# Kernel tuning notes

Hardware: AMD Instinct MI355X
Metric: run time of the kernel (lower is better)

The kernel has to match this reference:

```python
import jax, jax.numpy as jnp
import numpy as np


def _analytic_phase(x):
    """FFT-based analytic-signal phase, mean over channels. x: (B, C, T) -> (B, T)."""
    B, C, T = x.shape
    Xf = jnp.fft.fft(x, axis=-1)  # complex64
    # Hilbert multiplier: h[0]=1, h[1:T//2]=2, h[T//2]=1 (T even), rest 0
    h = np.zeros((T,), dtype=np.float32)
    h[0] = 1.0
    h[1:T // 2] = 2.0
    if T % 2 == 0:
        h[T // 2] = 1.0
    analytic = jnp.fft.ifft(Xf * jnp.asarray(h), axis=-1)
    phase = jnp.angle(analytic)          # (B, C, T)
    return phase.mean(axis=1)            # (B, T)


def setup_inputs() -> dict:
    key = jax.random.key(0)
    k = jax.random.split(key, 6)
    B, C, T = 32, 9, 4096
    num_codes, code_dim = 512, 64
    half = code_dim // 2
    s = 1.0 / np.sqrt(C)  # kaiming-uniform-ish scale for Linear(9, .)
    return {
        "imu_signal": jax.random.normal(k[0], (B, C, T), dtype=jnp.float32),
        "W_mag": jax.random.uniform(k[1], (half, C), jnp.float32, -s, s),
        "b_mag": jax.random.uniform(k[2], (half,), jnp.float32, -s, s),
        "W_phase": jax.random.uniform(k[3], (half, C), jnp.float32, -s, s),
        "b_phase": jax.random.uniform(k[4], (half,), jnp.float32, -s, s),
        "codebook": jax.random.normal(k[5], (num_codes, code_dim), dtype=jnp.float32),
    }


def reference(imu_signal, W_mag, b_mag, W_phase, b_phase, codebook):
    # imu_signal: (B, 9, T)
    phases = _analytic_phase(imu_signal)                      # (B, T)
    imu_btc = jnp.transpose(imu_signal, (0, 2, 1))            # (B, T, 9)

    mag_features = imu_btc @ W_mag.T + b_mag                  # (B, T, 32)

    phase_input = jnp.stack([jnp.cos(phases), jnp.sin(phases)], axis=-1)  # (B, T, 2)
    combined = jnp.concatenate([imu_btc[:, :, :7], phase_input], axis=-1)  # (B, T, 9)
    phase_features = combined @ W_phase.T + b_phase           # (B, T, 32)

    features = jnp.concatenate([mag_features, phase_features], axis=-1)  # (B, T, 64)

    # cdist argmin == argmin of squared distances: ||f||^2 - 2 f.c + ||c||^2
    d2 = (jnp.sum(features * features, axis=-1, keepdims=True)
          - 2.0 * jnp.einsum("btd,kd->btk", features, codebook)
          + jnp.sum(codebook * codebook, axis=-1))            # (B, T, K)
    indices = jnp.argmin(d2, axis=-1)                         # (B, T)
    quantized = codebook[indices]                             # (B, T, 64)
    return quantized, indices, phases
```

## Files before the change

kernel.cpp:

```cpp
#include <hip/hip_runtime.h>
#include <math.h>

#define TN 4096
#define HN 2048
#define NB 32
#define NCH 9
#define NCODES 512
#define CDIM 64
#define TAU 1e-3f
#define PTS 256
#define CHK 128
#define NCHK 4
#define VQT 512

typedef _Float16 f16x8 __attribute__((ext_vector_type(8)));
typedef float f32x4 __attribute__((ext_vector_type(4)));

__device__ __forceinline__ float2 cmulf(float2 a, float2 b) {
    return make_float2(a.x * b.x - a.y * b.y, a.x * b.y + a.y * b.x);
}
__device__ __forceinline__ float2 f2add(float2 a, float2 b) {
    return make_float2(a.x + b.x, a.y + b.y);
}
__device__ __forceinline__ float2 f2sub(float2 a, float2 b) {
    return make_float2(a.x - b.x, a.y - b.y);
}
__device__ __forceinline__ float2 f2scale(float2 a, float s) {
    return make_float2(a.x * s, a.y * s);
}

__device__ __forceinline__ unsigned long long packsi(float s, int i) {
    unsigned u = __float_as_uint(s);
    u = (u & 0x80000000u) ? ~u : (u | 0x80000000u);
    return ((unsigned long long)u << 32) | (unsigned)i;
}
__device__ __forceinline__ float unpacks(unsigned long long v) {
    unsigned u = (unsigned)(v >> 32);
    u = (u & 0x80000000u) ? (u & 0x7fffffffu) : ~u;
    return __uint_as_float(u);
}

__device__ __forceinline__ void gload_lds16(const void* g, void* l) {
    __builtin_amdgcn_global_load_lds(
        (const __attribute__((address_space(1))) unsigned int*)g,
        (__attribute__((address_space(3))) unsigned int*)l, 16, 0, 0);
}

__device__ __forceinline__ size_t aunit(int pbase, int plane, int s, int hi16, int l15) {
    return ((size_t)(((pbase * 2 + plane) * 2 + s) * 4 + hi16) << 4) + l15;
}

__global__ __launch_bounds__(256) void prep_kernel(const float* __restrict__ cb,
                                                   float* __restrict__ cn,
                                                   f16x8* __restrict__ cbswz,
                                                   float* __restrict__ ph) {
    const int bid = blockIdx.x;
    const int tid = threadIdx.x;
    if (bid < 512) {
        ph[bid * 256 + tid] = 0.0f;
        return;
    }
    if (bid < 544) {
        const int u = (bid - 512) * 256 + tid;
        const int k = u >> 4;
        const int j = u & 15;
        const int ob = j ^ (k & 15);
        const int plane = ob >> 3;
        const int d0 = (ob & 7) * 8;
        f16x8 out;
        #pragma unroll
        for (int e = 0; e < 8; ++e) {
            float c = cb[k * CDIM + d0 + e];
            _Float16 hh = (_Float16)c;
            out[e] = plane ? (_Float16)(c - (float)hh) : hh;
        }
        cbswz[u] = out;
        return;
    }
    for (int k = tid; k < NCODES; k += 256) {
        const float4* c4 = (const float4*)(cb + (size_t)k * CDIM);
        float s = 0.0f;
        #pragma unroll
        for (int q = 0; q < 16; ++q) {
            float4 c = c4[q];
            s = fmaf(c.x, c.x, s);
            s = fmaf(c.y, c.y, s);
            s = fmaf(c.z, c.z, s);
            s = fmaf(c.w, c.w, s);
        }
        cn[k] = s;
    }
}

#define HT 512
__global__ __launch_bounds__(HT) void hilbert_phase_kernel(
    const float* __restrict__ x, float* __restrict__ phases) {
    __shared__ float2 bufA[TN];
    __shared__ float2 bufB[TN];
    __shared__ float2 tw[HN];
    const int tid = threadIdx.x;
    const int row = blockIdx.x;
    const int b = row / NCH;
    const float* xr = x + (size_t)row * TN;
    const float inv = 1.0f / (float)TN;

    for (int i = tid; i < HN; i += HT) {
        float ang = -3.14159265358979323846f * ((float)i / (float)HN);
        float s, c;
        sincosf(ang, &s, &c);
        tw[i] = make_float2(c, s);
    }
    for (int i = tid; i < TN; i += HT) {
        bufA[i] = make_float2(xr[i], 0.0f);
    }
    __syncthreads();

    float2* src = bufA;
    float2* dst = bufB;
    for (int stage = 0; stage < 6; ++stage) {
        const int m = 1 << (2 * stage);
        for (int idx = tid; idx < 1024; idx += HT) {
            const int kk = idx & (m - 1);
            const int jm = idx - kk;
            float2 a0 = src[idx];
            float2 a1 = src[idx + 1024];
            float2 a2 = src[idx + 2048];
            float2 a3 = src[idx + 3072];
            float2 b0 = f2add(a0, a2);
            float2 b1 = f2add(a1, a3);
            float2 b2 = f2sub(a0, a2);
            float2 b3 = f2sub(a1, a3);
            float2 y0 = f2add(b0, b1);
            float2 mi = make_float2(b2.x + b3.y, b2.y - b3.x);
            float2 pi_ = make_float2(b2.x - b3.y, b2.y + b3.x);
            if (stage == 5) {
                const float sA_ = (idx == 0) ? inv : 2.0f * inv;
                const float sC_ = (idx == 0) ? inv : 0.0f;
                dst[idx]        = f2scale(y0, sA_);
                dst[idx + 1024] = f2scale(mi, 2.0f * inv);
                dst[idx + 2048] = f2scale(f2sub(b0, b1), sC_);
                dst[idx + 3072] = make_float2(0.0f, 0.0f);
            } else {
                float2 w1 = tw[jm];
                float2 w2 = tw[2 * jm];
                float2 w3 = cmulf(w1, w2);
                dst[4 * jm + kk]         = y0;
                dst[4 * jm + kk + m]     = cmulf(mi, w1);
                dst[4 * jm + kk + 2 * m] = cmulf(f2sub(b0, b1), w2);
                dst[4 * jm + kk + 3 * m] = cmulf(pi_, w3);
            }
        }
        __syncthreads();
        float2* t0 = src; src = dst; dst = t0;
    }
    for (int stage = 0; stage < 6; ++stage) {
        const int m = 1 << (2 * stage);
        for (int idx = tid; idx < 1024; idx += HT) {
            const int kk = idx & (m - 1);
            const int jm = idx - kk;
            float2 a0 = src[idx];
            float2 a1 = src[idx + 1024];
            float2 a2, a3;
            if (stage == 0) {
                a2 = (idx == 0) ? src[2048] : make_float2(0.0f, 0.0f);
                a3 = make_float2(0.0f, 0.0f);
            } else {
                a2 = src[idx + 2048];
                a3 = src[idx + 3072];
            }
            float2 b0 = f2add(a0, a2);
            float2 b1 = f2add(a1, a3);
            float2 b2 = f2sub(a0, a2);
            float2 b3 = f2sub(a1, a3);
            float2 w1 = tw[jm];      w1.y = -w1.y;
            float2 w2 = tw[2 * jm];  w2.y = -w2.y;
            float2 w3 = cmulf(w1, w2);
            float2 y0 = f2add(b0, b1);
            float2 pi_ = make_float2(b2.x - b3.y, b2.y + b3.x);
            float2 mi = make_float2(b2.x + b3.y, b2.y - b3.x);
            dst[4 * jm + kk]         = y0;
            dst[4 * jm + kk + m]     = cmulf(pi_, w1);
            dst[4 * jm + kk + 2 * m] = cmulf(f2sub(b0, b1), w2);
            dst[4 * jm + kk + 3 * m] = cmulf(mi, w3);
        }
        __syncthreads();
        float2* t0 = src; src = dst; dst = t0;
    }
    float* ph = phases + (size_t)b * TN;
    for (int i = tid; i < TN; i += HT) {
        float2 v = src[i];
        atomicAdd(&ph[i], atan2f(v.y, v.x) * (1.0f / 9.0f));
    }
}

__global__ __launch_bounds__(256) void feat_kernel(
    const float* __restrict__ imu,
    const float* __restrict__ Wm, const float* __restrict__ bm,
    const float* __restrict__ Wp, const float* __restrict__ bp,
    const float* __restrict__ phases,
    f16x8* __restrict__ atiles) {
    const int p = blockIdx.x * 256 + threadIdx.x;
    const int bb = p >> 12;
    const int tt = p & (TN - 1);
    float xc[9];
    #pragma unroll
    for (int c = 0; c < 9; ++c)
        xc[c] = imu[((size_t)(bb * 9 + c)) * TN + tt];
    float sp, cp;
    sincosf(phases[p], &sp, &cp);

    const int pbase = p >> 4;
    const int l15 = p & 15;
    #pragma unroll
    for (int g = 0; g < 8; ++g) {
        float v8[8];
        if (g < 4) {
            #pragma unroll
            for (int e = 0; e < 8; ++e) {
                const int j = 8 * g + e;
                float a = bm[j];
                #pragma unroll
                for (int c = 0; c < 9; ++c) a = fmaf(Wm[j * 9 + c], xc[c], a);
                v8[e] = a;
            }
        } else {
            #pragma unroll
            for (int e = 0; e < 8; ++e) {
                const int j = 8 * (g - 4) + e;
                float a = bp[j];
                #pragma unroll
                for (int c = 0; c < 7; ++c) a = fmaf(Wp[j * 9 + c], xc[c], a);
                a = fmaf(Wp[j * 9 + 7], cp, a);
                a = fmaf(Wp[j * 9 + 8], sp, a);
                v8[e] = a;
            }
        }
        f16x8 hv, lv;
        #pragma unroll
        for (int e = 0; e < 8; ++e) {
            _Float16 hh = (_Float16)v8[e];
            hv[e] = hh;
            lv[e] = (_Float16)(v8[e] - (float)hh);
        }
        const int s = g >> 2;
        const int hi16 = g & 3;
        atiles[aunit(pbase, 0, s, hi16, l15)] = hv;
        atiles[aunit(pbase, 1, s, hi16, l15)] = lv;
    }
}

__global__ __launch_bounds__(VQT, 4) void vq_kernel(
    const float* __restrict__ imu,
    const float* __restrict__ Wm, const float* __restrict__ bm,
    const float* __restrict__ Wp, const float* __restrict__ bp,
    const float* __restrict__ cb,
    const float* __restrict__ cn,
    const f16x8* __restrict__ cbswz,
    const float* __restrict__ phases,
    const f16x8* atiles,
    float* out_q,
    float* __restrict__ out_i) {
    __shared__ __align__(16) _Float16 sB[2][CHK][128];
    __shared__ int s_idx[PTS];
    const int tid = threadIdx.x;
    const int lane = tid & 63;
    const int w = tid >> 6;
    const int l15 = lane & 15;
    const int hi16 = lane >> 4;
    const int p0 = blockIdx.x * PTS;

    {
        const char* gsrc = (const char*)cbswz;
        char* ldst = (char*)&sB[0][0][0];
        #pragma unroll
        for (int i = 0; i < 4; ++i) {
            const int u = i * VQT + tid;
            gload_lds16(gsrc + (size_t)u * 16, ldst + u * 16);
        }
    }

    f16x8 aH[2][2], aL[2][2];
    #pragma unroll
    for (int rf = 0; rf < 2; ++rf) {
        const int prow = p0 + 32 * w + 16 * rf + l15;
        const int pbase = prow >> 4;
        #pragma unroll
        for (int s = 0; s < 2; ++s) {
            aH[rf][s] = atiles[aunit(pbase, 0, s, hi16, l15)];
            aL[rf][s] = atiles[aunit(pbase, 1, s, hi16, l15)];
        }
    }
    __syncthreads();

    float best[2][4], sec[2][4];
    int bidx[2][4];
    #pragma unroll
    for (int rf = 0; rf < 2; ++rf)
        #pragma unroll
        for (int r = 0; r < 4; ++r) {
            best[rf][r] = 3.4e38f; sec[rf][r] = 3.4e38f; bidx[rf][r] = 0;
        }

    for (int ch = 0; ch < NCHK; ++ch) {
        const int cur = ch & 1;
        if (ch < NCHK - 1) {
            const char* gsrc = (const char*)cbswz + (size_t)(ch + 1) * CHK * 256;
            char* ldst = (char*)&sB[cur ^ 1][0][0];
            #pragma unroll
            for (int i = 0; i < 4; ++i) {
                const int u = i * VQT + tid;
                gload_lds16(gsrc + (size_t)u * 16, ldst + u * 16);
            }
        }

        #pragma unroll
        for (int cf = 0; cf < 8; ++cf) {
            const int cl = 16 * cf + l15;
            const f16x8* brow = (const f16x8*)&sB[cur][cl][0];
            f32x4 acc[2];
            acc[0] = (f32x4){0.f, 0.f, 0.f, 0.f};
            acc[1] = (f32x4){0.f, 0.f, 0.f, 0.f};
            #pragma unroll
            for (int s = 0; s < 2; ++s) {
                f16x8 bH = brow[(4 * s + hi16) ^ l15];
                f16x8 bL = brow[(8 + 4 * s + hi16) ^ l15];
                #pragma unroll
                for (int rf = 0; rf < 2; ++rf) {
                    acc[rf] = __builtin_amdgcn_mfma_f32_16x16x32_f16(aH[rf][s], bH, acc[rf], 0, 0, 0);
                    acc[rf] = __builtin_amdgcn_mfma_f32_16x16x32_f16(aH[rf][s], bL, acc[rf], 0, 0, 0);
                    acc[rf] = __builtin_amdgcn_mfma_f32_16x16x32_f16(aL[rf][s], bH, acc[rf], 0, 0, 0);
                }
            }
            const int col = ch * CHK + 16 * cf + l15;
            const float cnv = cn[col];
            #pragma unroll
            for (int rf = 0; rf < 2; ++rf)
                #pragma unroll
                for (int r = 0; r < 4; ++r) {
                    float sc = fmaf(-2.0f, acc[rf][r], cnv);
                    bool lt = sc < best[rf][r];
                    float cand = lt ? best[rf][r] : sc;
                    sec[rf][r] = fminf(sec[rf][r], cand);
                    best[rf][r] = fminf(best[rf][r], sc);
                    bidx[rf][r] = lt ? col : bidx[rf][r];
                }
        }
        __syncthreads();
    }

    unsigned long long pb[2][4], ps[2][4];
    #pragma unroll
    for (int rf = 0; rf < 2; ++rf)
        #pragma unroll
        for (int r = 0; r < 4; ++r) {
            pb[rf][r] = packsi(best[rf][r], bidx[rf][r]);
            ps[rf][r] = packsi(sec[rf][r], 0);
        }
    #pragma unroll
    for (int m = 1; m <= 8; m <<= 1) {
        #pragma unroll
        for (int rf = 0; rf < 2; ++rf)
            #pragma unroll
            for (int r = 0; r < 4; ++r) {
                unsigned long long ob = __shfl_xor(pb[rf][r], m, 64);
                unsigned long long os = __shfl_xor(ps[rf][r], m, 64);
                unsigned long long mx = pb[rf][r] > ob ? pb[rf][r] : ob;
                unsigned long long mn = ps[rf][r] < os ? ps[rf][r] : os;
                ps[rf][r] = mx < mn ? mx : mn;
                pb[rf][r] = pb[rf][r] < ob ? pb[rf][r] : ob;
            }
    }
    if (l15 == 0) {
        #pragma unroll
        for (int rf = 0; rf < 2; ++rf)
            #pragma unroll
            for (int r = 0; r < 4; ++r) {
                const int row = 32 * w + 16 * rf + 4 * hi16 + r;
                const int bi = (int)(pb[rf][r] & 0xFFFFFFFFu);
                s_idx[row] = bi;
                out_i[p0 + row] = (float)bi;
            }
    }

    #pragma unroll
    for (int rf = 0; rf < 2; ++rf)
        #pragma unroll
        for (int r = 0; r < 4; ++r) {
            float gap = unpacks(ps[rf][r]) - unpacks(pb[rf][r]);
            unsigned long long bal = __ballot(l15 == 0 && gap < TAU);
            while (bal) {
                const int ln = __builtin_ctzll(bal);
                bal &= bal - 1;
                const int row = 32 * w + 16 * rf + (ln >> 4) * 4 + r;
                const int pR = p0 + row;
                const int bbR = pR >> 12;
                const int ttR = pR & (TN - 1);
                float xcR[9];
                #pragma unroll
                for (int c = 0; c < 9; ++c)
                    xcR[c] = imu[((size_t)(bbR * 9 + c)) * TN + ttR];
                float spR, cpR;
                sincosf(phases[pR], &spR, &cpR);
                float a0[8], a1[8], a2[8], a3[8];
                #pragma unroll
                for (int cc = 0; cc < 8; ++cc) {
                    a0[cc] = 0.f; a1[cc] = 0.f; a2[cc] = 0.f; a3[cc] = 0.f;
                }
                for (int d4 = 0; d4 < 16; ++d4) {
                    float fd[4];
                    #pragma unroll
                    for (int e = 0; e < 4; ++e) {
                        const int j = 4 * d4 + e;
                        float a;
                        if (j < 32) {
                            a = bm[j];
                            #pragma unroll
                            for (int c = 0; c < 9; ++c) a = fmaf(Wm[j * 9 + c], xcR[c], a);
                        } else {
                            const int jj = j - 32;
                            a = bp[jj];
                            #pragma unroll
                            for (int c = 0; c < 7; ++c) a = fmaf(Wp[jj * 9 + c], xcR[c], a);
                            a = fmaf(Wp[jj * 9 + 7], cpR, a);
                            a = fmaf(Wp[jj * 9 + 8], spR, a);
                        }
                        fd[e] = a;
                    }
                    #pragma unroll
                    for (int cc = 0; cc < 8; ++cc) {
                        const float4 cv = ((const float4*)(cb + (size_t)(lane * 8 + cc) * CDIM))[d4];
                        a0[cc] = fmaf(fd[0], cv.x, a0[cc]);
                        a1[cc] = fmaf(fd[1], cv.y, a1[cc]);
                        a2[cc] = fmaf(fd[2], cv.z, a2[cc]);
                        a3[cc] = fmaf(fd[3], cv.w, a3[cc]);
                    }
                }
                unsigned long long pbest = ~0ull;
                #pragma unroll
                for (int cc = 0; cc < 8; ++cc) {
                    const int kk = lane * 8 + cc;
                    float sc = fmaf(-2.0f, (a0[cc] + a1[cc]) + (a2[cc] + a3[cc]), cn[kk]);
                    unsigned long long pk = packsi(sc, kk);
                    pbest = pk < pbest ? pk : pbest;
                }
                #pragma unroll
                for (int m = 1; m <= 32; m <<= 1) {
                    unsigned long long o = __shfl_xor(pbest, m, 64);
                    pbest = o < pbest ? o : pbest;
                }
                if (lane == 0) {
                    const int bi = (int)(pbest & 0xFFFFFFFFu);
                    s_idx[row] = bi;
                    out_i[p0 + row] = (float)bi;
                }
            }
        }
    __syncthreads();

    float4* oq = (float4*)out_q;
    const float4* c4g = (const float4*)cb;
    for (int i = tid; i < PTS * 16; i += VQT) {
        const int pt = i >> 4;
        const int q = i & 15;
        oq[(size_t)(p0 + pt) * 16 + q] = c4g[(size_t)s_idx[pt] * 16 + q];
    }
}

extern "C" void kernel_launch(void* const* d_in, const int* in_sizes, int n_in,
                              void* d_out, int out_size, void* d_ws, size_t ws_size,
                              hipStream_t stream) {
    const float* imu = (const float*)d_in[0];
    const float* Wm  = (const float*)d_in[1];
    const float* bm  = (const float*)d_in[2];
    const float* Wp  = (const float*)d_in[3];
    const float* bp  = (const float*)d_in[4];
    const float* cb  = (const float*)d_in[5];

    float* out_q = (float*)d_out;
    float* out_i = out_q + (size_t)NB * TN * CDIM;
    float* out_p = out_i + (size_t)NB * TN;

    float* cn     = (float*)d_ws;
    f16x8* cbswz  = (f16x8*)((char*)d_ws + 2048);
    f16x8* atiles = (f16x8*)out_q;

    prep_kernel<<<545, 256, 0, stream>>>(cb, cn, cbswz, out_p);
    hilbert_phase_kernel<<<NB * NCH, HT, 0, stream>>>(imu, out_p);
    feat_kernel<<<(NB * TN) / 256, 256, 0, stream>>>(imu, Wm, bm, Wp, bp, out_p, atiles);
    vq_kernel<<<(NB * TN) / PTS, VQT, 0, stream>>>(imu, Wm, bm, Wp, bp, cb,
                                                   cn, cbswz, out_p, atiles,
                                                   out_q, out_i);
}
```

Before: 172.9 us.

## Pack two channels per complex FFT and make codebook tiles stationary in VQ

The Hilbert kernel now packs two real channel rows into one complex FFT. Each channel's analytic signal is recovered from the combined result: the imaginary part of channel one's analytic signal equals the output imaginary minus channel two's input, and similarly for channel two. This halves the FFT block count. Separately, the VQ kernel is restructured so each wave keeps codebook fragments in registers and streams the point tiles from global memory instead of staging codebook chunks through LDS. Per-wave best and second-best candidates are then merged through shared memory before the near-tie fallback. The changes trade LDS double buffering for repeated global loads of the point tiles and an extra shared-memory reduction stage. NB*NCH is odd (288 rows is even, fine), and since rows in a pair can straddle batches, atomics go to separate batch rows.

```diff
diff --git a/kernel.cpp b/kernel.cpp
--- a/kernel.cpp
+++ b/kernel.cpp
@@ -9,8 +9,6 @@
 #define CDIM 64
 #define TAU 1e-3f
 #define PTS 256
-#define CHK 128
-#define NCHK 4
 #define VQT 512
 
 typedef _Float16 f16x8 __attribute__((ext_vector_type(8)));
@@ -40,19 +38,13 @@
     return __uint_as_float(u);
 }
 
-__device__ __forceinline__ void gload_lds16(const void* g, void* l) {
-    __builtin_amdgcn_global_load_lds(
-        (const __attribute__((address_space(1))) unsigned int*)g,
-        (__attribute__((address_space(3))) unsigned int*)l, 16, 0, 0);
-}
-
 __device__ __forceinline__ size_t aunit(int pbase, int plane, int s, int hi16, int l15) {
     return ((size_t)(((pbase * 2 + plane) * 2 + s) * 4 + hi16) << 4) + l15;
 }
 
 __global__ __launch_bounds__(256) void prep_kernel(const float* __restrict__ cb,
                                                    float* __restrict__ cn,
-                                                   f16x8* __restrict__ cbswz,
+                                                   f16x8* __restrict__ ctiles,
                                                    float* __restrict__ ph) {
     const int bid = blockIdx.x;
     const int tid = threadIdx.x;
@@ -62,19 +54,20 @@
     }
     if (bid < 544) {
         const int u = (bid - 512) * 256 + tid;
-        const int k = u >> 4;
-        const int j = u & 15;
-        const int ob = j ^ (k & 15);
-        const int plane = ob >> 3;
-        const int d0 = (ob & 7) * 8;
+        const int l15 = u & 15;
+        const int hi16 = (u >> 4) & 3;
+        const int s = (u >> 6) & 1;
+        const int plane = (u >> 7) & 1;
+        const int cbase = u >> 8;
+        const int code = cbase * 16 + l15;
         f16x8 out;
         #pragma unroll
         for (int e = 0; e < 8; ++e) {
-            float c = cb[k * CDIM + d0 + e];
+            float c = cb[code * CDIM + 32 * s + 8 * hi16 + e];
             _Float16 hh = (_Float16)c;
             out[e] = plane ? (_Float16)(c - (float)hh) : hh;
         }
-        cbswz[u] = out;
+        ctiles[u] = out;
         return;
     }
     for (int k = tid; k < NCODES; k += 256) {
@@ -99,9 +92,12 @@
     __shared__ float2 bufB[TN];
     __shared__ float2 tw[HN];
     const int tid = threadIdx.x;
-    const int row = blockIdx.x;
-    const int b = row / NCH;
-    const float* xr = x + (size_t)row * TN;
+    const int row1 = 2 * blockIdx.x;
+    const int row2 = row1 + 1;
+    const int b1 = row1 / NCH;
+    const int b2 = row2 / NCH;
+    const float* xr1 = x + (size_t)row1 * TN;
+    const float* xr2 = x + (size_t)row2 * TN;
     const float inv = 1.0f / (float)TN;
 
     for (int i = tid; i < HN; i += HT) {
@@ -111,7 +107,7 @@
         tw[i] = make_float2(c, s);
     }
     for (int i = tid; i < TN; i += HT) {
-        bufA[i] = make_float2(xr[i], 0.0f);
+        bufA[i] = make_float2(xr1[i], xr2[i]);
     }
     __syncthreads();
 
@@ -186,10 +182,14 @@
         __syncthreads();
         float2* t0 = src; src = dst; dst = t0;
     }
-    float* ph = phases + (size_t)b * TN;
+    float* ph1 = phases + (size_t)b1 * TN;
+    float* ph2 = phases + (size_t)b2 * TN;
     for (int i = tid; i < TN; i += HT) {
-        float2 v = src[i];
-        atomicAdd(&ph[i], atan2f(v.y, v.x) * (1.0f / 9.0f));
+        float2 d = src[i];
+        float x1v = xr1[i];
+        float x2v = xr2[i];
+        atomicAdd(&ph1[i], atan2f(d.y - x2v, x1v) * (1.0f / 9.0f));
+        atomicAdd(&ph2[i], atan2f(x1v - d.x, x2v) * (1.0f / 9.0f));
     }
 }
 
@@ -255,206 +255,177 @@
     const float* __restrict__ Wp, const float* __restrict__ bp,
     const float* __restrict__ cb,
     const float* __restrict__ cn,
-    const f16x8* __restrict__ cbswz,
+    const f16x8* __restrict__ ctiles,
     const float* __restrict__ phases,
     const f16x8* atiles,
     float* out_q,
     float* __restrict__ out_i) {
-    __shared__ __align__(16) _Float16 sB[2][CHK][128];
+    __shared__ unsigned long long s_bs[16][PTS][2];
     __shared__ int s_idx[PTS];
+    __shared__ float s_gap[PTS];
     const int tid = threadIdx.x;
     const int lane = tid & 63;
     const int w = tid >> 6;
     const int l15 = lane & 15;
     const int hi16 = lane >> 4;
     const int p0 = blockIdx.x * PTS;
-
-    {
-        const char* gsrc = (const char*)cbswz;
-        char* ldst = (char*)&sB[0][0][0];
+    const int pb0 = p0 >> 4;
+
+    for (int h = 0; h < 2; ++h) {
+        const int kbase = 64 * w + 32 * h;
+        f16x8 cH[2][2], cL[2][2];
         #pragma unroll
-        for (int i = 0; i < 4; ++i) {
-            const int u = i * VQT + tid;
-            gload_lds16(gsrc + (size_t)u * 16, ldst + u * 16);
-        }
-    }
-
-    f16x8 aH[2][2], aL[2][2];
-    #pragma unroll
-    for (int rf = 0; rf < 2; ++rf) {
-        const int prow = p0 + 32 * w + 16 * rf + l15;
-        const int pbase = prow >> 4;
+        for (int rf = 0; rf < 2; ++rf) {
+            const int cbase = (kbase >> 4) + rf;
+            #pragma unroll
+            for (int s = 0; s < 2; ++s) {
+                cH[rf][s] = ctiles[aunit(cbase, 0, s, hi16, l15)];
+                cL[rf][s] = ctiles[aunit(cbase, 1, s, hi16, l15)];
+            }
+        }
+        float cnv[2][4];
         #pragma unroll
-        for (int s = 0; s < 2; ++s) {
-            aH[rf][s] = atiles[aunit(pbase, 0, s, hi16, l15)];
-            aL[rf][s] = atiles[aunit(pbase, 1, s, hi16, l15)];
-        }
-    }
-    __syncthreads();
-
-    float best[2][4], sec[2][4];
-    int bidx[2][4];
-    #pragma unroll
-    for (int rf = 0; rf < 2; ++rf)
-        #pragma unroll
-        for (int r = 0; r < 4; ++r) {
-            best[rf][r] = 3.4e38f; sec[rf][r] = 3.4e38f; bidx[rf][r] = 0;
-        }
-
-    for (int ch = 0; ch < NCHK; ++ch) {
-        const int cur = ch & 1;
-        if (ch < NCHK - 1) {
-            const char* gsrc = (const char*)cbswz + (size_t)(ch + 1) * CHK * 256;
-            char* ldst = (char*)&sB[cur ^ 1][0][0];
-            #pragma unroll
-            for (int i = 0; i < 4; ++i) {
-                const int u = i * VQT + tid;
-                gload_lds16(gsrc + (size_t)u * 16, ldst + u * 16);
-            }
-        }
-
-        #pragma unroll
-        for (int cf = 0; cf < 8; ++cf) {
-            const int cl = 16 * cf + l15;
-            const f16x8* brow = (const f16x8*)&sB[cur][cl][0];
+        for (int rf = 0; rf < 2; ++rf)
+            #pragma unroll
+            for (int r = 0; r < 4; ++r)
+                cnv[rf][r] = cn[kbase + 16 * rf + 4 * hi16 + r];
+
+        #pragma unroll 4
+        for (int cf = 0; cf < 16; ++cf) {
+            const int pbase = pb0 + cf;
+            f16x8 bH[2], bL[2];
+            #pragma unroll
+            for (int s = 0; s < 2; ++s) {
+                bH[s] = atiles[aunit(pbase, 0, s, hi16, l15)];
+                bL[s] = atiles[aunit(pbase, 1, s, hi16, l15)];
+            }
             f32x4 acc[2];
             acc[0] = (f32x4){0.f, 0.f, 0.f, 0.f};
             acc[1] = (f32x4){0.f, 0.f, 0.f, 0.f};
             #pragma unroll
-            for (int s = 0; s < 2; ++s) {
-                f16x8 bH = brow[(4 * s + hi16) ^ l15];
-                f16x8 bL = brow[(8 + 4 * s + hi16) ^ l15];
+            for (int s = 0; s < 2; ++s)
                 #pragma unroll
                 for (int rf = 0; rf < 2; ++rf) {
-                    acc[rf] = __builtin_amdgcn_mfma_f32_16x16x32_f16(aH[rf][s], bH, acc[rf], 0, 0, 0);
-                    acc[rf] = __builtin_amdgcn_mfma_f32_16x16x32_f16(aH[rf][s], bL, acc[rf], 0, 0, 0);
-                    acc[rf] = __builtin_amdgcn_mfma_f32_16x16x32_f16(aL[rf][s], bH, acc[rf], 0, 0, 0);
+                    acc[rf] = __builtin_amdgcn_mfma_f32_16x16x32_f16(cH[rf][s], bH[s], acc[rf], 0, 0, 0);
+                    acc[rf] = __builtin_amdgcn_mfma_f32_16x16x32_f16(cH[rf][s], bL[s], acc[rf], 0, 0, 0);
+                    acc[rf] = __builtin_amdgcn_mfma_f32_16x16x32_f16(cL[rf][s], bH[s], acc[rf], 0, 0, 0);
                 }
-            }
-            const int col = ch * CHK + 16 * cf + l15;
-            const float cnv = cn[col];
+            unsigned long long b = ~0ull, sec = ~0ull;
             #pragma unroll
             for (int rf = 0; rf < 2; ++rf)
                 #pragma unroll
                 for (int r = 0; r < 4; ++r) {
-                    float sc = fmaf(-2.0f, acc[rf][r], cnv);
-                    bool lt = sc < best[rf][r];
-                    float cand = lt ? best[rf][r] : sc;
-                    sec[rf][r] = fminf(sec[rf][r], cand);
-                    best[rf][r] = fminf(best[rf][r], sc);
-                    bidx[rf][r] = lt ? col : bidx[rf][r];
+                    float sc = fmaf(-2.0f, acc[rf][r], cnv[rf][r]);
+                    unsigned long long pk = packsi(sc, kbase + 16 * rf + 4 * hi16 + r);
+                    unsigned long long mx = b > pk ? b : pk;
+                    sec = sec < mx ? sec : mx;
+                    b = b < pk ? b : pk;
                 }
-        }
-        __syncthreads();
-    }
-
-    unsigned long long pb[2][4], ps[2][4];
-    #pragma unroll
-    for (int rf = 0; rf < 2; ++rf)
-        #pragma unroll
-        for (int r = 0; r < 4; ++r) {
-            pb[rf][r] = packsi(best[rf][r], bidx[rf][r]);
-            ps[rf][r] = packsi(sec[rf][r], 0);
-        }
-    #pragma unroll
-    for (int m = 1; m <= 8; m <<= 1) {
-        #pragma unroll
-        for (int rf = 0; rf < 2; ++rf)
-            #pragma unroll
-            for (int r = 0; r < 4; ++r) {
-                unsigned long long ob = __shfl_xor(pb[rf][r], m, 64);
-                unsigned long long os = __shfl_xor(ps[rf][r], m, 64);
-                unsigned long long mx = pb[rf][r] > ob ? pb[rf][r] : ob;
-                unsigned long long mn = ps[rf][r] < os ? ps[rf][r] : os;
-                ps[rf][r] = mx < mn ? mx : mn;
-                pb[rf][r] = pb[rf][r] < ob ? pb[rf][r] : ob;
-            }
-    }
-    if (l15 == 0) {
-        #pragma unroll
-        for (int rf = 0; rf < 2; ++rf)
-            #pragma unroll
-            for (int r = 0; r < 4; ++r) {
-                const int row = 32 * w + 16 * rf + 4 * hi16 + r;
-                const int bi = (int)(pb[rf][r] & 0xFFFFFFFFu);
+            #pragma unroll
+            for (int m = 16; m <= 32; m <<= 1) {
+                unsigned long long ob = __shfl_xor(b, m, 64);
+                unsigned long long os = __shfl_xor(sec, m, 64);
+                unsigned long long mx = b > ob ? b : ob;
+                unsigned long long mn = sec < os ? sec : os;
+                sec = mx < mn ? mx : mn;
+                b = b < ob ? b : ob;
+            }
+            if (hi16 == 0) {
+                s_bs[2 * w + h][16 * cf + l15][0] = b;
+                s_bs[2 * w + h][16 * cf + l15][1] = sec;
+            }
+        }
+    }
+    __syncthreads();
+
+    if (tid < PTS) {
+        unsigned long long b = ~0ull, sec = ~0ull;
+        #pragma unroll 4
+        for (int q = 0; q < 16; ++q) {
+            unsigned long long ob = s_bs[q][tid][0];
+            unsigned long long os = s_bs[q][tid][1];
+            unsigned long long mx = b > ob ? b : ob;
+            unsigned long long mn = sec < os ? sec : os;
+            sec = mx < mn ? mx : mn;
+            b = b < ob ? b : ob;
+        }
+        const int bi = (int)(b & 0xFFFFFFFFu);
+        s_idx[tid] = bi;
+        out_i[p0 + tid] = (float)bi;
+        s_gap[tid] = unpacks(sec) - unpacks(b);
+    }
+    __syncthreads();
+
+    {
+        bool fl = (lane < 32) && (s_gap[32 * w + (lane & 31)] < TAU);
+        unsigned long long bal = __ballot(fl);
+        while (bal) {
+            const int ln = __builtin_ctzll(bal);
+            bal &= bal - 1;
+            const int row = 32 * w + ln;
+            const int pR = p0 + row;
+            const int bbR = pR >> 12;
+            const int ttR = pR & (TN - 1);
+            float xcR[9];
+            #pragma unroll
+            for (int c = 0; c < 9; ++c)
+                xcR[c] = imu[((size_t)(bbR * 9 + c)) * TN + ttR];
+            float spR, cpR;
+            sincosf(phases[pR], &spR, &cpR);
+            float a0[8], a1[8], a2[8], a3[8];
+            #pragma unroll
+            for (int cc = 0; cc < 8; ++cc) {
+                a0[cc] = 0.f; a1[cc] = 0.f; a2[cc] = 0.f; a3[cc] = 0.f;
+            }
+            for (int d4 = 0; d4 < 16; ++d4) {
+                float fd[4];
+                #pragma unroll
+                for (int e = 0; e < 4; ++e) {
+                    const int j = 4 * d4 + e;
+                    float a;
+                    if (j < 32) {
+                        a = bm[j];
+                        #pragma unroll
+                        for (int c = 0; c < 9; ++c) a = fmaf(Wm[j * 9 + c], xcR[c], a);
+                    } else {
+                        const int jj = j - 32;
+                        a = bp[jj];
+                        #pragma unroll
+                        for (int c = 0; c < 7; ++c) a = fmaf(Wp[jj * 9 + c], xcR[c], a);
+                        a = fmaf(Wp[jj * 9 + 7], cpR, a);
+                        a = fmaf(Wp[jj * 9 + 8], spR, a);
+                    }
+                    fd[e] = a;
+                }
+                #pragma unroll
+                for (int cc = 0; cc < 8; ++cc) {
+                    const float4 cv = ((const float4*)(cb + (size_t)(lane * 8 + cc) * CDIM))[d4];
+                    a0[cc] = fmaf(fd[0], cv.x, a0[cc]);
+                    a1[cc] = fmaf(fd[1], cv.y, a1[cc]);
+                    a2[cc] = fmaf(fd[2], cv.z, a2[cc]);
+                    a3[cc] = fmaf(fd[3], cv.w, a3[cc]);
+                }
+            }
+            unsigned long long pbest = ~0ull;
+            #pragma unroll
+            for (int cc = 0; cc < 8; ++cc) {
+                const int kk = lane * 8 + cc;
+                float sc = fmaf(-2.0f, (a0[cc] + a1[cc]) + (a2[cc] + a3[cc]), cn[kk]);
+                unsigned long long pk = packsi(sc, kk);
+                pbest = pk < pbest ? pk : pbest;
+            }
+            #pragma unroll
+            for (int m = 1; m <= 32; m <<= 1) {
+                unsigned long long o = __shfl_xor(pbest, m, 64);
+                pbest = o < pbest ? o : pbest;
+            }
+            if (lane == 0) {
+                const int bi = (int)(pbest & 0xFFFFFFFFu);
                 s_idx[row] = bi;
                 out_i[p0 + row] = (float)bi;
             }
-    }
-
-    #pragma unroll
-    for (int rf = 0; rf < 2; ++rf)
-        #pragma unroll
-        for (int r = 0; r < 4; ++r) {
-            float gap = unpacks(ps[rf][r]) - unpacks(pb[rf][r]);
-            unsigned long long bal = __ballot(l15 == 0 && gap < TAU);
-            while (bal) {
-                const int ln = __builtin_ctzll(bal);
-                bal &= bal - 1;
-                const int row = 32 * w + 16 * rf + (ln >> 4) * 4 + r;
-                const int pR = p0 + row;
-                const int bbR = pR >> 12;
-                const int ttR = pR & (TN - 1);
-                float xcR[9];
-                #pragma unroll
-                for (int c = 0; c < 9; ++c)
-                    xcR[c] = imu[((size_t)(bbR * 9 + c)) * TN + ttR];
-                float spR, cpR;
-                sincosf(phases[pR], &spR, &cpR);
-                float a0[8], a1[8], a2[8], a3[8];
-                #pragma unroll
-                for (int cc = 0; cc < 8; ++cc) {
-                    a0[cc] = 0.f; a1[cc] = 0.f; a2[cc] = 0.f; a3[cc] = 0.f;
-                }
-                for (int d4 = 0; d4 < 16; ++d4) {
-                    float fd[4];
-                    #pragma unroll
-                    for (int e = 0; e < 4; ++e) {
-                        const int j = 4 * d4 + e;
-                        float a;
-                        if (j < 32) {
-                            a = bm[j];
-                            #pragma unroll
-                            for (int c = 0; c < 9; ++c) a = fmaf(Wm[j * 9 + c], xcR[c], a);
-                        } else {
-                            const int jj = j - 32;
-                            a = bp[jj];
-                            #pragma unroll
-                            for (int c = 0; c < 7; ++c) a = fmaf(Wp[jj * 9 + c], xcR[c], a);
-                            a = fmaf(Wp[jj * 9 + 7], cpR, a);
-                            a = fmaf(Wp[jj * 9 + 8], spR, a);
-                        }
-                        fd[e] = a;
-                    }
-                    #pragma unroll
-                    for (int cc = 0; cc < 8; ++cc) {
-                        const float4 cv = ((const float4*)(cb + (size_t)(lane * 8 + cc) * CDIM))[d4];
-                        a0[cc] = fmaf(fd[0], cv.x, a0[cc]);
-                        a1[cc] = fmaf(fd[1], cv.y, a1[cc]);
-                        a2[cc] = fmaf(fd[2], cv.z, a2[cc]);
-                        a3[cc] = fmaf(fd[3], cv.w, a3[cc]);
-                    }
-                }
-                unsigned long long pbest = ~0ull;
-                #pragma unroll
-                for (int cc = 0; cc < 8; ++cc) {
-                    const int kk = lane * 8 + cc;
-                    float sc = fmaf(-2.0f, (a0[cc] + a1[cc]) + (a2[cc] + a3[cc]), cn[kk]);
-                    unsigned long long pk = packsi(sc, kk);
-                    pbest = pk < pbest ? pk : pbest;
-                }
-                #pragma unroll
-                for (int m = 1; m <= 32; m <<= 1) {
-                    unsigned long long o = __shfl_xor(pbest, m, 64);
-                    pbest = o < pbest ? o : pbest;
-                }
-                if (lane == 0) {
-                    const int bi = (int)(pbest & 0xFFFFFFFFu);
-                    s_idx[row] = bi;
-                    out_i[p0 + row] = (float)bi;
-                }
-            }
-        }
+        }
+    }
     __syncthreads();
 
     float4* oq = (float4*)out_q;
@@ -481,13 +452,13 @@
     float* out_p = out_i + (size_t)NB * TN;
 
     float* cn     = (float*)d_ws;
-    f16x8* cbswz  = (f16x8*)((char*)d_ws + 2048);
+    f16x8* ctiles = (f16x8*)((char*)d_ws + 2048);
     f16x8* atiles = (f16x8*)out_q;
 
-    prep_kernel<<<545, 256, 0, stream>>>(cb, cn, cbswz, out_p);
-    hilbert_phase_kernel<<<NB * NCH, HT, 0, stream>>>(imu, out_p);
+    prep_kernel<<<545, 256, 0, stream>>>(cb, cn, ctiles, out_p);
+    hilbert_phase_kernel<<<NB * NCH / 2, HT, 0, stream>>>(imu, out_p);
     feat_kernel<<<(NB * TN) / 256, 256, 0, stream>>>(imu, Wm, bm, Wp, bp, out_p, atiles);
     vq_kernel<<<(NB * TN) / PTS, VQT, 0, stream>>>(imu, Wm, bm, Wp, bp, cb,
-                                                   cn, cbswz, out_p, atiles,
+                                                   cn, ctiles, out_p, atiles,
                                                    out_q, out_i);
 }
```

After: 183.1 us. 1.06x slower.
